# Kernel optimization log

Hardware: AMD Instinct MI355X
Metric: run time of the kernel (lower is better)

Reference implementation:

```python
import jax, jax.numpy as jnp
import numpy as np

B, N, C = 8, 6000, 21            # batch, proposals (pre_nms_topn), total_labels
VARIANCES = jnp.array([0.1, 0.1, 0.2, 0.2], jnp.float32)
MAX_TOTAL = 200                   # max_total_size == max_output_size_per_class
SCORE_THR = 0.5
IOU_THR = 0.5                     # tf combined_non_max_suppression default
NEG = -1e9                        # finite sentinel for suppressed scores


def setup_inputs() -> dict:
    key = jax.random.key(0)
    k1, k2, k3, k4 = jax.random.split(key, 4)
    # valid normalized rois: y1,x1 in [0,0.8), positive height/width
    yx1 = jax.random.uniform(k1, (B, N, 2), jnp.float32) * 0.8
    hw = jax.random.uniform(k4, (B, N, 2), jnp.float32) * 0.2 + 0.01
    roi_bboxes = jnp.concatenate([yx1, yx1 + hw], axis=-1)  # [B,N,4] y1x1y2x2
    pred_deltas = jax.random.normal(k2, (B, N, C * 4), jnp.float32) * 0.5
    pred_label_probs = jax.random.uniform(k3, (B, N, C), jnp.float32)
    return {"roi_bboxes": roi_bboxes, "pred_deltas": pred_deltas,
            "pred_label_probs": pred_label_probs}


def reference(roi_bboxes, pred_deltas, pred_label_probs):
    # --- bbox delta decoding ---
    deltas = pred_deltas.reshape(B, N, C, 4) * VARIANCES          # [B,N,C,4]
    roi = roi_bboxes[:, :, None, :]                               # [B,N,1,4]
    anc_h = roi[..., 2] - roi[..., 0]
    anc_w = roi[..., 3] - roi[..., 1]
    anc_cy = roi[..., 0] + 0.5 * anc_h
    anc_cx = roi[..., 1] + 0.5 * anc_w
    bh = jnp.exp(deltas[..., 2]) * anc_h
    bw = jnp.exp(deltas[..., 3]) * anc_w
    bcy = deltas[..., 0] * anc_h + anc_cy
    bcx = deltas[..., 1] * anc_w + anc_cx
    y1 = bcy - 0.5 * bh
    x1 = bcx - 0.5 * bw
    y2 = y1 + bh
    x2 = x1 + bw
    boxes = jnp.stack([y1, x1, y2, x2], axis=-1)                  # [B,N,C,4]
    boxes = jnp.clip(boxes, 0.0, 1.0)  # combined NMS clip_boxes=True default

    # zero out scores where argmax class is background (0)
    lbl = jnp.argmax(pred_label_probs, axis=-1)                   # [B,N]
    scores = jnp.where((lbl != 0)[..., None], pred_label_probs, 0.0)

    boxes = boxes.transpose(0, 2, 1, 3)                           # [B,C,N,4]
    scores = scores.transpose(0, 2, 1)                            # [B,C,N]
    s0 = jnp.where(scores > SCORE_THR, scores, NEG)

    areas = (jnp.maximum(boxes[..., 2] - boxes[..., 0], 0.0) *
             jnp.maximum(boxes[..., 3] - boxes[..., 1], 0.0))     # [B,C,N]

    # --- greedy per-class NMS, vectorized over (B,C) ---
    def step(s, _):
        idx = jnp.argmax(s, axis=-1)                              # [B,C]
        val = jnp.take_along_axis(s, idx[..., None], axis=-1)[..., 0]
        box = jnp.take_along_axis(boxes, idx[..., None, None], axis=2)[..., 0, :]
        valid = val > NEG * 0.5
        iy1 = jnp.maximum(box[..., None, 0], boxes[..., 0])
        ix1 = jnp.maximum(box[..., None, 1], boxes[..., 1])
        iy2 = jnp.minimum(box[..., None, 2], boxes[..., 2])
        ix2 = jnp.minimum(box[..., None, 3], boxes[..., 3])
        inter = jnp.maximum(iy2 - iy1, 0.0) * jnp.maximum(ix2 - ix1, 0.0)
        sel_a = (jnp.maximum(box[..., 2] - box[..., 0], 0.0) *
                 jnp.maximum(box[..., 3] - box[..., 1], 0.0))
        iou = inter / (sel_a[..., None] + areas - inter + 1e-8)   # [B,C,N]
        s = jnp.where((iou > IOU_THR) & valid[..., None], NEG, s)
        return s, (box, val, valid)

    _, (sel_box, sel_val, sel_ok) = jax.lax.scan(step, s0, None, length=MAX_TOTAL)
    # [T,B,C,*] -> [B, C*T, *]
    sel_box = sel_box.transpose(1, 2, 0, 3).reshape(B, C * MAX_TOTAL, 4)
    sel_val = sel_val.transpose(1, 2, 0).reshape(B, C * MAX_TOTAL)
    sel_ok = sel_ok.transpose(1, 2, 0).reshape(B, C * MAX_TOTAL)
    cls = jnp.broadcast_to(jnp.arange(C, dtype=jnp.float32)[None, :, None],
                           (B, C, MAX_TOTAL)).reshape(B, C * MAX_TOTAL)

    sel_val = jnp.where(sel_ok, sel_val, NEG)
    top_s, top_i = jax.lax.top_k(sel_val, MAX_TOTAL)              # [B,200]
    fb = jnp.take_along_axis(sel_box, top_i[..., None], axis=1)
    fc = jnp.take_along_axis(cls, top_i, axis=1)
    ok = top_s > NEG * 0.5
    final_scores = jnp.where(ok, top_s, 0.0)
    final_bboxes = jnp.where(ok[..., None], fb, 0.0)
    final_labels = jnp.where(ok, fc, 0.0)
    return final_bboxes, final_labels, final_scores
```

## Files before the change

kernel.cpp:

```cpp
#include <hip/hip_runtime.h>

#define B_    8
#define N_    6000
#define C_    21
#define MAXT  200
#define NEGV  -1000000000.0f
#define UCAP  4096
#define CCAP  1024
#define CTGT  512
#define NBUCK 64
#define NTH   1024
#define NENT  (C_ * MAXT)
#define NBLK  (B_ * C_)


__device__ __forceinline__ unsigned ford(float f) {
  unsigned u = __float_as_uint(f);
  return (u & 0x80000000u) ? ~u : (u | 0x80000000u);
}
__device__ __forceinline__ float funord(unsigned o) {
  unsigned u = (o & 0x80000000u) ? (o ^ 0x80000000u) : ~o;
  return __uint_as_float(u);
}

__device__ __forceinline__ float4 decode_box(const float* __restrict__ roi,
                                             const float* __restrict__ deltas,
                                             int b, int n, int c)
{
#pragma clang fp contract(off)
  float4 r = *(const float4*)(roi + ((size_t)b * N_ + n) * 4);
  float4 d = *(const float4*)(deltas + ((size_t)b * N_ + n) * (C_ * 4) + c * 4);
  float d0 = d.x * 0.1f, d1 = d.y * 0.1f, d2 = d.z * 0.2f, d3 = d.w * 0.2f;
  float ah = r.z - r.x, aw = r.w - r.y;
  float acy = r.x + 0.5f * ah, acx = r.y + 0.5f * aw;
  float bh = expf(d2) * ah, bw = expf(d3) * aw;
  float bcy = d0 * ah + acy, bcx = d1 * aw + acx;
  float y1 = bcy - 0.5f * bh, x1 = bcx - 0.5f * bw;
  float y2 = y1 + bh, x2 = x1 + bw;
  y1 = fminf(fmaxf(y1, 0.f), 1.f); x1 = fminf(fmaxf(x1, 0.f), 1.f);
  y2 = fminf(fmaxf(y2, 0.f), 1.f); x2 = fminf(fmaxf(x2, 0.f), 1.f);
  return make_float4(y1, x1, y2, x2);
}

__device__ __forceinline__ float area_ref(float4 s) {
#pragma clang fp contract(off)
  return fmaxf(s.z - s.x, 0.f) * fmaxf(s.w - s.y, 0.f);
}

__device__ __forceinline__ float iou_pre(float4 s, float sa, float4 o, float oa) {
#pragma clang fp contract(off)
  float iy1 = fmaxf(s.x, o.x), ix1 = fmaxf(s.y, o.y);
  float iy2 = fminf(s.z, o.z), ix2 = fminf(s.w, o.w);
  float inter = fmaxf(iy2 - iy1, 0.f) * fmaxf(ix2 - ix1, 0.f);
  return inter / (sa + oa - inter + 1e-08f);
}

struct Smem {
  unsigned long long ukeys[UCAP];
  unsigned long long cbuf[CCAP];
  float4 cboxAll[512];
  float4 comm[MAXT];
  float careaAll[512];
  float commA[MAXT];
  unsigned long long kill[64];
  unsigned long long s_dead[16];
  int hist[NBUCK];
  int ctr[NBUCK];
  int wcnt[16];
  int s_cnt, s_clen, s_ncomm, s_blo, s_len, s_m, s_mx;
};

__global__ __launch_bounds__(256) void prep_kernel(
    const float* __restrict__ probs, float* __restrict__ probsT)
{
  int t = blockIdx.x * 256 + threadIdx.x;
  if (t >= B_ * N_) return;
  int b = t / N_, n = t - b * N_;
  const float* pr = probs + (size_t)t * C_;
  float p[C_];
  #pragma unroll
  for (int k = 0; k < C_; ++k) p[k] = pr[k];
  float mx = p[0]; int am = 0;
  #pragma unroll
  for (int k = 1; k < C_; ++k) { if (p[k] > mx) { mx = p[k]; am = k; } }
  float msk = (am != 0) ? 1.0f : 0.0f;
  #pragma unroll
  for (int c = 0; c < C_; ++c)
    probsT[((size_t)b * C_ + c) * N_ + n] = p[c] * msk;
}

__global__ __launch_bounds__(NTH) void nms_kernel(
    const float* __restrict__ roi, const float* __restrict__ deltas,
    const float* __restrict__ probs, const float* __restrict__ probsT,
    float* __restrict__ sel_val, float* __restrict__ sel_box)
{
#pragma clang fp contract(off)
  __shared__ Smem sm;
  const int bc = blockIdx.x, b = bc / C_, c = bc % C_;
  const int tid = threadIdx.x, lane = tid & 63, wv = tid >> 6;

  if (tid < NBUCK) sm.hist[tid] = 0;
  if (tid == 0) { sm.s_cnt = 0; sm.s_ncomm = 0; }
  __syncthreads();

  int M;
  const float* rowT = probsT ? (probsT + (size_t)bc * N_) : nullptr;
  if (rowT) {
    float scv[6];
    #pragma unroll
    for (int it = 0; it < 6; ++it) {
      int n = it * NTH + tid;
      scv[it] = (n < N_) ? rowT[n] : 0.f;
    }
    int off[6];
    int wtot = 0;
    #pragma unroll
    for (int it = 0; it < 6; ++it) {
      bool cand = (scv[it] > 0.5f);
      unsigned long long m = __ballot(cand);
      off[it] = wtot + __popcll(m & ((1ULL << lane) - 1ULL));
      wtot += __popcll(m);
    }
    if (lane == 0) sm.wcnt[wv] = wtot;
    __syncthreads();
    int wbase = 0, mtot = 0;
    #pragma unroll
    for (int w = 0; w < 16; ++w) {
      int t2 = sm.wcnt[w];
      if (w < wv) wbase += t2;
      mtot += t2;
    }
    #pragma unroll
    for (int it = 0; it < 6; ++it) {
      if (scv[it] > 0.5f) {
        int pos = wbase + off[it];
        if (pos < UCAP) {
          unsigned hi = ford(scv[it]);
          int n = it * NTH + tid;
          sm.ukeys[pos] = ((unsigned long long)hi << 32) |
                          (unsigned)(0xFFFFFFFFu - (unsigned)n);
          atomicAdd(&sm.hist[(hi >> 17) & (NBUCK - 1)], 1);
        }
      }
    }
    __syncthreads();
    M = mtot < UCAP ? mtot : UCAP;
  } else {
    for (int base0 = 0; base0 < N_; base0 += NTH) {
      int n = base0 + tid;
      bool cand = false;
      float sc = 0.f;
      if (n < N_) {
        const float* pr = probs + ((size_t)b * N_ + n) * C_;
        float mx = pr[0]; int am = 0;
        #pragma unroll
        for (int k = 1; k < C_; ++k) { float v = pr[k]; if (v > mx) { mx = v; am = k; } }
        if (am != 0) sc = pr[c];
        cand = (sc > 0.5f);
      }
      unsigned long long m = __ballot(cand);
      int wcnt2 = __popcll(m);
      int bslot = 0;
      if (lane == 0 && wcnt2) bslot = atomicAdd(&sm.s_cnt, wcnt2);
      bslot = __shfl(bslot, 0);
      if (cand) {
        int pos = bslot + __popcll(m & ((1ULL << lane) - 1ULL));
        if (pos < UCAP) {
          unsigned hi = ford(sc);
          sm.ukeys[pos] = ((unsigned long long)hi << 32) |
                          (unsigned)(0xFFFFFFFFu - (unsigned)n);
          atomicAdd(&sm.hist[(hi >> 17) & (NBUCK - 1)], 1);
        }
      }
    }
    __syncthreads();
    M = sm.s_cnt < UCAP ? sm.s_cnt : UCAP;
  }

  float* sv = sel_val + (size_t)bc * MAXT;
  float* sb = sel_box + (size_t)bc * MAXT * 4;

  int bhi = NBUCK - 1;
  while (true) {
    if (sm.s_ncomm >= MAXT || bhi < 0) break;

    if (wv == 0) {
      int h = (lane <= bhi) ? sm.hist[bhi - lane] : 0;
      int p = h;
      #pragma unroll
      for (int d = 1; d < 64; d <<= 1) {
        int o = __shfl_up(p, d);
        if (lane >= d) p += o;
      }
      unsigned long long ok = __ballot(p <= CTGT);
      int m = __popcll(ok);
      if (m == 0) m = 1;
      if (m > bhi + 1) m = bhi + 1;
      int len = __shfl(p, m - 1);
      if (lane < m) sm.ctr[bhi - lane] = p - h;
      int hv = (lane < m) ? h : 0;
      #pragma unroll
      for (int d = 1; d < 64; d <<= 1) hv = max(hv, __shfl_xor(hv, d));
      if (lane == 0) {
        sm.s_blo = bhi - (m - 1); sm.s_len = len; sm.s_clen = 0;
        sm.s_m = m; sm.s_mx = hv;
      }
    }
    __syncthreads();
    int blo = sm.s_blo;
    if (sm.s_len == 0) break;
    int mbk = sm.s_m, mxb = sm.s_mx;

    for (int i = tid; i < M; i += NTH) {
      unsigned long long kk = sm.ukeys[i];
      int bk = (int)((kk >> 49) & (NBUCK - 1));
      if (bk >= blo && bk <= bhi) {
        int slot = atomicAdd(&sm.ctr[bk], 1);
        if (slot < CCAP) sm.cbuf[slot] = kk;
      }
    }
    __syncthreads();
    int alen = sm.s_len < CCAP ? sm.s_len : CCAP;

    if (alen > 0) {
      if (alen <= 512 && mxb <= 128) {
        for (int j = wv; j < mbk; j += 16) {
          int bk = bhi - j;
          int len = sm.hist[bk];
          if (len <= 0) continue;
          int base = sm.ctr[bk] - len;
          if (len <= 64) {
            unsigned long long v = (lane < len) ? sm.cbuf[base + lane] : 0ULL;
            #pragma unroll
            for (int k = 2; k <= 64; k <<= 1) {
              for (int jj = k >> 1; jj > 0; jj >>= 1) {
                unsigned long long w = __shfl_xor(v, jj);
                bool takeMax = ((lane & jj) == 0) == ((lane & k) == 0);
                if ((w > v) == takeMax) v = w;
              }
            }
            if (lane < len) sm.cbuf[base + lane] = v;
          } else {
            unsigned long long v0 = (lane < len) ? sm.cbuf[base + lane] : 0ULL;
            unsigned long long v1 = (64 + lane < len) ? sm.cbuf[base + 64 + lane] : 0ULL;
            #pragma unroll
            for (int k = 2; k <= 128; k <<= 1) {
              for (int jj = k >> 1; jj > 0; jj >>= 1) {
                if (jj == 64) {
                  unsigned long long a = (v0 > v1) ? v0 : v1;
                  unsigned long long bmin = (v0 > v1) ? v1 : v0;
                  v0 = a; v1 = bmin;
                } else {
                  unsigned long long w0 = __shfl_xor(v0, jj);
                  unsigned long long w1 = __shfl_xor(v1, jj);
                  bool e0k = ((lane & k) == 0);
                  bool e1k = (((lane + 64) & k) == 0);
                  bool jz = ((lane & jj) == 0);
                  bool tm0 = (jz == e0k);
                  bool tm1 = (jz == e1k);
                  if ((w0 > v0) == tm0) v0 = w0;
                  if ((w1 > v1) == tm1) v1 = w1;
                }
              }
            }
            if (lane < len) sm.cbuf[base + lane] = v0;
            if (64 + lane < len) sm.cbuf[base + 64 + lane] = v1;
          }
        }
        __syncthreads();
      } else {
        int SORTP = 64;
        while (SORTP < alen) SORTP <<= 1;
        unsigned long long v = (tid < alen) ? sm.cbuf[tid] : 0ULL;
        for (int k = 2; k <= SORTP; k <<= 1) {
          for (int j = k >> 1; j > 0; j >>= 1) {
            bool takeMax = ((tid & j) == 0) == ((tid & k) == 0);
            unsigned long long w;
            if (j >= 64) {
              __syncthreads(); if (tid < SORTP) sm.cbuf[tid] = v; __syncthreads();
              w = sm.cbuf[tid ^ j];
            } else {
              w = __shfl_xor(v, j);
            }
            if (tid < SORTP && (w > v) == takeMax) v = w;
          }
        }
        __syncthreads();
        if (tid < SORTP) sm.cbuf[tid] = v;
        __syncthreads();
      }

      if (tid < alen && tid < 512) {
        int n = (int)(0xFFFFFFFFu - (unsigned)(sm.cbuf[tid] & 0xFFFFFFFFull));
        float4 bb = decode_box(roi, deltas, b, n, c);
        sm.cboxAll[tid] = bb;
        sm.careaAll[tid] = area_ref(bb);
      }
      __syncthreads();

      int start = 0;
      int wlen = alen < 512 ? alen : 512;
      while (true) {
        int nc = sm.s_ncomm;
        if (nc >= MAXT || start >= wlen) break;
        int bs = min(64, wlen - start);

        float4 ib = sm.cboxAll[start + lane];
        float ia = sm.careaAll[start + lane];
        #pragma unroll
        for (int r = 0; r < 4; ++r) {
          int j = (wv << 2) | r;
          float4 jb4 = sm.cboxAll[start + j];
          float ja = sm.careaAll[start + j];
          bool kf = (j < bs) && (lane < bs) && (lane > j) &&
                    (iou_pre(jb4, ja, ib, ia) > 0.5f);
          unsigned long long rowm = __ballot(kf);
          if (lane == 0) sm.kill[j] = rowm;
        }
        {
          bool dead = false;
          if (lane < bs) {
            for (int jc = wv; jc < nc; jc += 16) {
              if (iou_pre(sm.comm[jc], sm.commA[jc], ib, ia) > 0.5f) { dead = true; break; }
            }
          }
          unsigned long long dm = __ballot(dead);
          if (lane == 0) sm.s_dead[wv] = dm;
        }
        __syncthreads();

        if (wv == 0) {
          unsigned long long sup = sm.s_dead[0];
          #pragma unroll
          for (int w2 = 1; w2 < 16; ++w2) sup |= sm.s_dead[w2];
          unsigned long long row = sm.kill[lane];
          #pragma unroll
          for (int s5 = 0; s5 < 6; ++s5) {
            const unsigned long long Ms[6] = {
              0x5555555555555555ULL, 0x3333333333333333ULL,
              0x0F0F0F0F0F0F0F0FULL, 0x00FF00FF00FF00FFULL,
              0x0000FFFF0000FFFFULL, 0x00000000FFFFFFFFULL };
            int d = 1 << s5;
            unsigned long long other = __shfl_xor(row, d);
            unsigned long long Mk = Ms[s5];
            row = ((lane & d) == 0) ? ((row & Mk) | ((other & Mk) << d))
                                    : ((row & ~Mk) | ((other & ~Mk) >> d));
          }
          unsigned long long col = row;

          unsigned long long alive = ~sup;
          if (bs < 64) alive &= (1ULL << bs) - 1ULL;
          unsigned long long pend = alive, chosen = 0ULL;
          while (pend) {
            bool rdy_b = ((col & pend) == 0ULL);
            unsigned long long rdy = __ballot(rdy_b) & pend;
            bool kld_b = ((col & chosen) != 0ULL);
            unsigned long long kl = __ballot(kld_b);
            chosen |= rdy & ~kl;
            pend &= ~rdy;
          }
          int take = MAXT - nc;
          if (__popcll(chosen) > take) {
            bool keep = ((chosen >> lane) & 1ULL) &&
                        (__popcll(chosen & ((1ULL << lane) - 1ULL)) < take);
            chosen = __ballot(keep);
          }
          if ((chosen >> lane) & 1ULL) {
            int rnk = nc + __popcll(chosen & ((1ULL << lane) - 1ULL));
            float4 bb2 = sm.cboxAll[start + lane];
            sm.comm[rnk] = bb2;
            sm.commA[rnk] = sm.careaAll[start + lane];
            sv[rnk] = funord((unsigned)(sm.cbuf[start + lane] >> 32));
            sb[(size_t)rnk * 4 + 0] = bb2.x; sb[(size_t)rnk * 4 + 1] = bb2.y;
            sb[(size_t)rnk * 4 + 2] = bb2.z; sb[(size_t)rnk * 4 + 3] = bb2.w;
          }
          if (lane == 0) sm.s_ncomm = nc + __popcll(chosen);
        }
        __syncthreads();
        start += bs;
      }
    }
    bhi = blo - 1;
  }

  int T = sm.s_ncomm;
  for (int j2 = T + tid; j2 < MAXT; j2 += NTH) sv[j2] = NEGV;
}

__global__ __launch_bounds__(NTH) void merge2_kernel(
    const float* __restrict__ sel_val, const float* __restrict__ sel_box,
    float* __restrict__ out)
{
  __shared__ Smem sm;
  const int bc = blockIdx.x;
  const int b = bc / C_, sc = bc % C_;
  const int tid = threadIdx.x;
  int* s_rank = reinterpret_cast<int*>(sm.cboxAll);

  for (int i = tid; i < NENT; i += NTH) {
    float v = sel_val[(size_t)b * NENT + i];
    unsigned long long key = ((unsigned long long)ford(v) << 32) |
                             (unsigned)(0xFFFFFFFFu - (unsigned)i);
    if (i < UCAP) sm.ukeys[i] = key; else sm.cbuf[i - UCAP] = key;
  }
  if (tid < MAXT) s_rank[tid] = 0;
  __syncthreads();

  auto klds = [&](int i) -> unsigned long long {
    return (i < UCAP) ? sm.ukeys[i] : sm.cbuf[i - UCAP];
  };

  if (tid < 1000) {
    int q = tid / MAXT, t = tid - q * MAXT;
    int e = sc * MAXT + t;
    unsigned long long mykey = klds(e);
    int part = 0;
    for (int cc = q; cc < C_; cc += 5) {
      int lo = 0, hi = MAXT;
      while (lo < hi) {
        int mid = (lo + hi) >> 1;
        if (klds(cc * MAXT + mid) > mykey) lo = mid + 1; else hi = mid;
      }
      part += lo;
    }
    atomicAdd(&s_rank[t], part);
  }
  __syncthreads();

  if (tid < MAXT) {
    int t = tid;
    int e = sc * MAXT + t;
    int rank = s_rank[t];
    if (rank < MAXT) {
      float* obx = out + (size_t)b * MAXT * 4;
      float* olb = out + (size_t)B_ * MAXT * 4 + (size_t)b * MAXT;
      float* osc = out + (size_t)B_ * MAXT * 5 + (size_t)b * MAXT;
      float v = funord((unsigned)(klds(e) >> 32));
      if (v > NEGV * 0.5f) {
        osc[rank] = v;
        olb[rank] = (float)sc;
        const float* bp = sel_box + ((size_t)b * NENT + e) * 4;
        obx[rank * 4 + 0] = bp[0]; obx[rank * 4 + 1] = bp[1];
        obx[rank * 4 + 2] = bp[2]; obx[rank * 4 + 3] = bp[3];
      } else {
        osc[rank] = 0.f; olb[rank] = 0.f;
        obx[rank * 4 + 0] = 0.f; obx[rank * 4 + 1] = 0.f;
        obx[rank * 4 + 2] = 0.f; obx[rank * 4 + 3] = 0.f;
      }
    }
  }
}

extern "C" void kernel_launch(void* const* d_in, const int* in_sizes, int n_in,
                              void* d_out, int out_size, void* d_ws, size_t ws_size,
                              hipStream_t stream)
{
  const float* roi    = (const float*)d_in[0];
  const float* deltas = (const float*)d_in[1];
  const float* probs  = (const float*)d_in[2];
  float* out = (float*)d_out;
  float* ws  = (float*)d_ws;

  float* sel_val = ws;
  float* sel_box = ws + (size_t)B_ * NENT;
  float* probsT  = ws + (size_t)B_ * NENT * 5;
  size_t need_mid = ((size_t)B_ * NENT * 5 + (size_t)B_ * C_ * N_) * sizeof(float);
  bool haveT = (ws_size >= need_mid);

  const float* probsT_arg = haveT ? probsT : nullptr;
  if (haveT)
    prep_kernel<<<dim3((B_ * N_ + 255) / 256), dim3(256), 0, stream>>>(probs, probsT);
  nms_kernel<<<dim3(NBLK), dim3(NTH), 0, stream>>>(
      roi, deltas, probs, probsT_arg, sel_val, sel_box);
  merge2_kernel<<<dim3(NBLK), dim3(NTH), 0, stream>>>(sel_val, sel_box, out);
}
```

Before: 96.10 us.

## Fuse box decode into bucket sort and precompute all intra-batch kill masks

The per-bucket wavefront sort now decodes boxes and areas right after writing each sorted key, removing a separate decode pass and its barrier. The intra-batch IoU kill-mask computation is hoisted out of the sequential selection loop into an upfront pass that fills masks for all 64-wide batches. This takes work off the serial critical path, where each iteration is followed by a block barrier. In exchange, masks are computed for batches the loop may never reach once 200 boxes are chosen, and more shared memory is used.

```diff
diff --git a/kernel.cpp b/kernel.cpp
--- a/kernel.cpp
+++ b/kernel.cpp
@@ -62,7 +62,7 @@
   float4 comm[MAXT];
   float careaAll[512];
   float commA[MAXT];
-  unsigned long long kill[64];
+  unsigned long long killAll[8][64];
   unsigned long long s_dead[16];
   int hist[NBUCK];
   int ctr[NBUCK];
@@ -239,7 +239,13 @@
                 if ((w > v) == takeMax) v = w;
               }
             }
-            if (lane < len) sm.cbuf[base + lane] = v;
+            if (lane < len) {
+              sm.cbuf[base + lane] = v;
+              int n = (int)(0xFFFFFFFFu - (unsigned)(v & 0xFFFFFFFFull));
+              float4 bb = decode_box(roi, deltas, b, n, c);
+              sm.cboxAll[base + lane] = bb;
+              sm.careaAll[base + lane] = area_ref(bb);
+            }
           } else {
             unsigned long long v0 = (lane < len) ? sm.cbuf[base + lane] : 0ULL;
             unsigned long long v1 = (64 + lane < len) ? sm.cbuf[base + 64 + lane] : 0ULL;
@@ -263,8 +269,20 @@
                 }
               }
             }
-            if (lane < len) sm.cbuf[base + lane] = v0;
-            if (64 + lane < len) sm.cbuf[base + 64 + lane] = v1;
+            if (lane < len) {
+              sm.cbuf[base + lane] = v0;
+              int n = (int)(0xFFFFFFFFu - (unsigned)(v0 & 0xFFFFFFFFull));
+              float4 bb = decode_box(roi, deltas, b, n, c);
+              sm.cboxAll[base + lane] = bb;
+              sm.careaAll[base + lane] = area_ref(bb);
+            }
+            if (64 + lane < len) {
+              sm.cbuf[base + 64 + lane] = v1;
+              int n = (int)(0xFFFFFFFFu - (unsigned)(v1 & 0xFFFFFFFFull));
+              float4 bb = decode_box(roi, deltas, b, n, c);
+              sm.cboxAll[base + 64 + lane] = bb;
+              sm.careaAll[base + 64 + lane] = area_ref(bb);
+            }
           }
         }
         __syncthreads();
@@ -288,18 +306,38 @@
         __syncthreads();
         if (tid < SORTP) sm.cbuf[tid] = v;
         __syncthreads();
-      }
-
-      if (tid < alen && tid < 512) {
-        int n = (int)(0xFFFFFFFFu - (unsigned)(sm.cbuf[tid] & 0xFFFFFFFFull));
-        float4 bb = decode_box(roi, deltas, b, n, c);
-        sm.cboxAll[tid] = bb;
-        sm.careaAll[tid] = area_ref(bb);
-      }
-      __syncthreads();
-
-      int start = 0;
+        if (tid < alen && tid < 512) {
+          int n = (int)(0xFFFFFFFFu - (unsigned)(sm.cbuf[tid] & 0xFFFFFFFFull));
+          float4 bb = decode_box(roi, deltas, b, n, c);
+          sm.cboxAll[tid] = bb;
+          sm.careaAll[tid] = area_ref(bb);
+        }
+        __syncthreads();
+      }
+
       int wlen = alen < 512 ? alen : 512;
+
+      {
+        int nbat = (wlen + 63) >> 6;
+        for (int bi = 0; bi < nbat; ++bi) {
+          int bst = bi << 6;
+          int bs = min(64, wlen - bst);
+          float4 ib = sm.cboxAll[bst + lane];
+          float ia = sm.careaAll[bst + lane];
+          #pragma unroll
+          for (int r = 0; r < 4; ++r) {
+            int j = (wv << 2) | r;
+            float4 jb4 = sm.cboxAll[bst + j];
+            float ja = sm.careaAll[bst + j];
+            bool kf = (j < bs) && (lane < bs) && (lane > j) &&
+                      (iou_pre(jb4, ja, ib, ia) > 0.5f);
+            unsigned long long rowm = __ballot(kf);
+            if (lane == 0) sm.killAll[bi][j] = rowm;
+          }
+        }
+      }
+
+      int start = 0, bi = 0;
       while (true) {
         int nc = sm.s_ncomm;
         if (nc >= MAXT || start >= wlen) break;
@@ -307,16 +345,6 @@
 
         float4 ib = sm.cboxAll[start + lane];
         float ia = sm.careaAll[start + lane];
-        #pragma unroll
-        for (int r = 0; r < 4; ++r) {
-          int j = (wv << 2) | r;
-          float4 jb4 = sm.cboxAll[start + j];
-          float ja = sm.careaAll[start + j];
-          bool kf = (j < bs) && (lane < bs) && (lane > j) &&
-                    (iou_pre(jb4, ja, ib, ia) > 0.5f);
-          unsigned long long rowm = __ballot(kf);
-          if (lane == 0) sm.kill[j] = rowm;
-        }
         {
           bool dead = false;
           if (lane < bs) {
@@ -333,7 +361,7 @@
           unsigned long long sup = sm.s_dead[0];
           #pragma unroll
           for (int w2 = 1; w2 < 16; ++w2) sup |= sm.s_dead[w2];
-          unsigned long long row = sm.kill[lane];
+          unsigned long long row = sm.killAll[bi][lane];
           #pragma unroll
           for (int s5 = 0; s5 < 6; ++s5) {
             const unsigned long long Ms[6] = {
@@ -377,7 +405,7 @@
           if (lane == 0) sm.s_ncomm = nc + __popcll(chosen);
         }
         __syncthreads();
-        start += bs;
+        start += bs; ++bi;
       }
     }
     bhi = blo - 1;
```

Measured after the change: 100.9 us. 1.05x slower.
